# Kernel tuning notes

Measured on AMD Instinct MI355X. Metric: run time of the kernel, lower is better.

The kernel has to match this reference:

```python
import jax, jax.numpy as jnp
import numpy as np

NEG = -1e30

def setup_inputs() -> dict:
    key = jax.random.key(0)
    ks = jax.random.split(key, 11)
    B, NA, NB = 8, 2048, 2048
    in_A, in_B, out_dim = 256, 256, 64
    s = 0.05
    return {
        "h_A": jax.random.normal(ks[0], (B, NA, in_A), jnp.float32),
        "h_B": jax.random.normal(ks[1], (B, NB, in_B), jnp.float32),
        "mask": jax.random.bernoulli(ks[2], 0.5, (B, NA, NB)),
        "WA_w": jax.random.normal(ks[3], (in_A, out_dim), jnp.float32) * s,
        "WA_b": jax.random.normal(ks[4], (out_dim,), jnp.float32) * s,
        "WB_w": jax.random.normal(ks[5], (in_B, out_dim), jnp.float32) * s,
        "WB_b": jax.random.normal(ks[6], (out_dim,), jnp.float32) * s,
        "aA_w": jax.random.normal(ks[7], (out_dim,), jnp.float32) * s,
        "aA_b": jax.random.normal(ks[8], (), jnp.float32) * s,
        "aB_w": jax.random.normal(ks[9], (out_dim,), jnp.float32) * s,
        "aB_b": jax.random.normal(ks[10], (), jnp.float32) * s,
    }

def reference(h_A, h_B, mask, WA_w, WA_b, WB_w, WB_b, aA_w, aA_b, aB_w, aB_b):
    # Linear projections: z_A [B,NA,D], z_B [B,NB,D]
    z_A = jnp.einsum('bnd,df->bnf', h_A, WA_w) + WA_b
    z_B = jnp.einsum('bmd,df->bmf', h_B, WB_w) + WB_b
    # Additive attention scores: [B,NA,1] + [B,1,NB] -> [B,NA,NB]
    sA = z_A @ aA_w + aA_b  # [B,NA]
    sB = z_B @ aB_w + aB_b  # [B,NB]
    e = sA[:, :, None] + sB[:, None, :]
    e = jnp.where(mask, e, NEG)
    e = jax.nn.leaky_relu(e, negative_slope=0.01)
    alpha = jax.nn.softmax(e, axis=-1)
    alpha = jnp.where(mask, alpha, 0.0)
    # Weighted sum over neighbors
    return jnp.einsum('bnm,bmf->bnf', alpha, z_B)
```

## Files before the change

kernel.cpp:

```cpp
#include <hip/hip_runtime.h>

typedef short bf16x8 __attribute__((ext_vector_type(8)));
typedef float f32x4 __attribute__((ext_vector_type(4)));

__device__ __forceinline__ unsigned short f2bf(float x) {
  unsigned u = __float_as_uint(x);
  u += 0x7FFFu + ((u >> 16) & 1u);
  return (unsigned short)(u >> 16);
}
__device__ __forceinline__ float bf2f(unsigned short h) {
  return __uint_as_float(((unsigned)h) << 16);
}

__device__ __forceinline__ float wave_reduce_sum(float v) {
  #pragma unroll
  for (int off = 1; off < 64; off <<= 1) v += __shfl_xor(v, off, 64);
  return v;
}

__global__ void prep_kernel(const float* __restrict__ WA_w, const float* __restrict__ WA_b,
                            const float* __restrict__ aA_w, const float* __restrict__ aA_b,
                            const float* __restrict__ WB_w,
                            const unsigned char* __restrict__ mask8,
                            float* __restrict__ vA, float* __restrict__ cA,
                            unsigned short* __restrict__ WBT, int* __restrict__ mflag) {
  if (blockIdx.x < 64) {
    const int f = blockIdx.x, k = threadIdx.x;
    WBT[f * 256 + k] = f2bf(WB_w[k * 64 + f]);
    return;
  }
  const int t = threadIdx.x;
  const unsigned v = mask8[t * 4 + 1];
  const unsigned long long bal = __ballot(v != 0);
  __shared__ unsigned red[4];
  const int wave = t >> 6, lane = t & 63;
  if (lane == 0) red[wave] = (bal != 0ull) ? 1u : 0u;
  float sa = 0.f;
  for (int ff = 0; ff < 64; ++ff) sa += WA_w[t * 64 + ff] * aA_w[ff];
  vA[t] = sa;
  __syncthreads();
  if (t == 0) {
    float ca = aA_b[0];
    for (int ff = 0; ff < 64; ++ff) ca += WA_b[ff] * aA_w[ff];
    cA[0] = ca;
    mflag[0] = (red[0] | red[1] | red[2] | red[3]) ? 1 : 0;
  }
}

__global__ __launch_bounds__(256) void zB_kernel(
    const float* __restrict__ hB, const unsigned short* __restrict__ WBT,
    const float* __restrict__ WB_b, const float* __restrict__ aB_w,
    const float* __restrict__ aB_b,
    unsigned short* __restrict__ zBT, float* __restrict__ sB,
    float* __restrict__ msB_blk) {
  __shared__ char hl[32768];
  __shared__ char wt[32768];
  __shared__ float red16[16];
  const int t = threadIdx.x, w = t >> 6, l = t & 63;
  const int q = l >> 4, ln = l & 15;
  const int r0 = blockIdx.x * 64;
  const int b = r0 >> 11;
  const int mloc = r0 & 2047;

  {
    const int f = t >> 2, c = t & 3;
    const unsigned short* src = WBT + f * 256;
    #pragma unroll
    for (int j = 0; j < 8; ++j) {
      const int k8 = c + j * 4;
      bf16x8 v = *(const bf16x8*)(src + k8 * 8);
      *(bf16x8*)(wt + ((f * 512 + k8 * 16) ^ ((f & 7) << 4))) = v;
    }
  }
  {
    const int row = t >> 2, seg = t & 3;
    const float* src = hB + (size_t)(r0 + row) * 256 + seg * 64;
    #pragma unroll
    for (int i = 0; i < 8; ++i) {
      float4 x = *(const float4*)(src + i * 8);
      float4 y = *(const float4*)(src + i * 8 + 4);
      bf16x8 v;
      v[0] = (short)f2bf(x.x); v[1] = (short)f2bf(x.y);
      v[2] = (short)f2bf(x.z); v[3] = (short)f2bf(x.w);
      v[4] = (short)f2bf(y.x); v[5] = (short)f2bf(y.y);
      v[6] = (short)f2bf(y.z); v[7] = (short)f2bf(y.w);
      *(bf16x8*)(hl + ((row * 512 + seg * 128 + i * 16) ^ ((row & 7) << 4))) = v;
    }
  }
  __syncthreads();
  f32x4 acc[4];
  #pragma unroll
  for (int nr = 0; nr < 4; ++nr) acc[nr] = (f32x4){0.f, 0.f, 0.f, 0.f};
  const int rowA = w * 16 + ln;
  #pragma unroll
  for (int kk = 0; kk < 8; ++kk) {
    const int ko = kk * 64 + q * 16;
    bf16x8 a = *(const bf16x8*)(hl + ((rowA * 512 + ko) ^ ((rowA & 7) << 4)));
    #pragma unroll
    for (int nr = 0; nr < 4; ++nr) {
      const int f = nr * 16 + ln;
      bf16x8 bb = *(const bf16x8*)(wt + ((f * 512 + ko) ^ ((f & 7) << 4)));
      acc[nr] = __builtin_amdgcn_mfma_f32_16x16x32_bf16(a, bb, acc[nr], 0, 0, 0);
    }
  }
  float z[4][4];
  float p[4] = {0.f, 0.f, 0.f, 0.f};
  #pragma unroll
  for (int nr = 0; nr < 4; ++nr) {
    const int f = nr * 16 + ln;
    const float bias = WB_b[f];
    const float aw = aB_w[f];
    #pragma unroll
    for (int r = 0; r < 4; ++r) {
      const float zz = acc[nr][r] + bias;
      z[nr][r] = zz;
      p[r] += zz * aw;
    }
  }
  #pragma unroll
  for (int r = 0; r < 4; ++r) {
    #pragma unroll
    for (int off = 1; off < 16; off <<= 1) p[r] += __shfl_xor(p[r], off, 16);
  }
  if (ln == 0) {
    const float cb = aB_b[0];
    float lm = -1e30f;
    #pragma unroll
    for (int r = 0; r < 4; ++r) {
      const float s = p[r] + cb;
      sB[r0 + w * 16 + q * 4 + r] = s;
      lm = fmaxf(lm, s);
    }
    red16[w * 4 + q] = lm;
  }
  __syncthreads();
  if (t == 0) {
    float bm = red16[0];
    #pragma unroll
    for (int i = 1; i < 16; ++i) bm = fmaxf(bm, red16[i]);
    msB_blk[blockIdx.x] = bm;
  }
  #pragma unroll
  for (int nr = 0; nr < 4; ++nr) {
    const int f = nr * 16 + ln;
    uint2 pk;
    pk.x = (unsigned)f2bf(z[nr][0]) | ((unsigned)f2bf(z[nr][1]) << 16);
    pk.y = (unsigned)f2bf(z[nr][2]) | ((unsigned)f2bf(z[nr][3]) << 16);
    *(uint2*)(hl + ((f * 128 + (w * 16 + q * 4) * 2) ^ ((f & 7) << 4))) = pk;
  }
  __syncthreads();
  {
    const int sf = t >> 3, sm8 = t & 7;
    #pragma unroll
    for (int i = 0; i < 2; ++i) {
      const int f = sf + i * 32;
      bf16x8 v = *(const bf16x8*)(hl + ((f * 128 + sm8 * 16) ^ ((f & 7) << 4)));
      *(bf16x8*)(zBT + (size_t)b * 131072 + f * 2048 + mloc + sm8 * 8) = v;
    }
  }
}

__global__ __launch_bounds__(256) void gat_kernel(
    const unsigned short* __restrict__ zBT, const float* __restrict__ hA,
    const float* __restrict__ vA, const float* __restrict__ cA,
    const float* __restrict__ sB, const float* __restrict__ msB_blk,
    const unsigned char* __restrict__ mask8, const int* __restrict__ mask32,
    const int* __restrict__ mflag, float* __restrict__ out) {
  const int b = blockIdx.y;
  const int n0 = blockIdx.x * 32;
  const int t = threadIdx.x;
  const int w = t >> 6, l = t & 63;
  const int q = l >> 4, ln = l & 15;
  const bool use8 = (*mflag != 0);

  __shared__ char zbl[2][16384];
  __shared__ char wl[2][8192];
  __shared__ float sAl[32];
  __shared__ float dl[32];

  const float4 vA4 = ((const float4*)vA)[l];
  const float cA0 = cA[0];
  #pragma unroll
  for (int r = 0; r < 8; ++r) {
    const int row = w * 8 + r;
    const float4 h4 = *(const float4*)(hA + ((size_t)(b * 2048 + n0 + row)) * 256 + l * 4);
    float s = h4.x * vA4.x + h4.y * vA4.y + h4.z * vA4.z + h4.w * vA4.w;
    s = wave_reduce_sum(s);
    if (l == 0) sAl[row] = s + cA0;
  }
  float mb = -1e30f;
  #pragma unroll 8
  for (int i = 0; i < 32; ++i) mb = fmaxf(mb, msB_blk[b * 32 + i]);
  __syncthreads();

  const int n2 = t >> 4;
  const int m8 = t & 15;
  const float sA0 = sAl[n2], sA1 = sAl[n2 + 16];
  const float M0f = sA0 + mb, M1f = sA1 + mb;
  const float M0 = M0f >= 0.f ? M0f : 0.01f * M0f;
  const float M1 = M1f >= 0.f ? M1f : 0.01f * M1f;
  float ds0 = 0.f, ds1 = 0.f;
  f32x4 acc0 = (f32x4){0.f, 0.f, 0.f, 0.f}, acc1 = acc0;

  const unsigned short* zb = zBT + (size_t)b * 131072;
  const size_t mrow0 = ((size_t)(b * 2048 + n0 + n2)) * 2048 + m8 * 8;
  const size_t mrow1 = mrow0 + (size_t)16 * 2048;
  const int zf = t >> 2, zseg = t & 3;
  const int fB = w * 16 + ln;
  const int wbyte0 = (n2 * 256 + m8 * 16) ^ ((n2 & 7) << 4);
  const int wbyte1 = ((n2 + 16) * 256 + m8 * 16) ^ (((n2 + 16) & 7) << 4);

  for (int mt = 0; mt < 16; ++mt) {
    const int m0 = mt * 128;
    char* zc = zbl[mt & 1];
    char* wc = wl[mt & 1];
    bf16x8 zv[4];
    #pragma unroll
    for (int i = 0; i < 4; ++i)
      zv[i] = *(const bf16x8*)(zb + zf * 2048 + m0 + zseg * 32 + i * 8);
    const float4 s0 = *(const float4*)(sB + b * 2048 + m0 + m8 * 8);
    const float4 s1 = *(const float4*)(sB + b * 2048 + m0 + m8 * 8 + 4);
    const float sbx[8] = {s0.x, s0.y, s0.z, s0.w, s1.x, s1.y, s1.z, s1.w};
    int k0[8], k1[8];
    if (use8) {
      const uint2 a = *(const uint2*)(mask8 + mrow0 + m0);
      const uint2 c = *(const uint2*)(mask8 + mrow1 + m0);
      #pragma unroll
      for (int j = 0; j < 4; ++j) {
        k0[j] = (a.x >> (8 * j)) & 0xFF; k0[j + 4] = (a.y >> (8 * j)) & 0xFF;
        k1[j] = (c.x >> (8 * j)) & 0xFF; k1[j + 4] = (c.y >> (8 * j)) & 0xFF;
      }
    } else {
      const int4 a = *(const int4*)(mask32 + mrow0 + m0);
      const int4 a2 = *(const int4*)(mask32 + mrow0 + m0 + 4);
      const int4 c = *(const int4*)(mask32 + mrow1 + m0);
      const int4 c2 = *(const int4*)(mask32 + mrow1 + m0 + 4);
      k0[0] = a.x; k0[1] = a.y; k0[2] = a.z; k0[3] = a.w;
      k0[4] = a2.x; k0[5] = a2.y; k0[6] = a2.z; k0[7] = a2.w;
      k1[0] = c.x; k1[1] = c.y; k1[2] = c.z; k1[3] = c.w;
      k1[4] = c2.x; k1[5] = c2.y; k1[6] = c2.z; k1[7] = c2.w;
    }
    unsigned short wb0[8], wb1[8];
    #pragma unroll
    for (int j = 0; j < 8; ++j) {
      const float x0 = sA0 + sbx[j];
      const float e0 = x0 >= 0.f ? x0 : 0.01f * x0;
      const float v0 = k0[j] ? __expf(e0 - M0) : 0.f;
      wb0[j] = f2bf(v0); ds0 += bf2f(wb0[j]);
      const float x1 = sA1 + sbx[j];
      const float e1 = x1 >= 0.f ? x1 : 0.01f * x1;
      const float v1 = k1[j] ? __expf(e1 - M1) : 0.f;
      wb1[j] = f2bf(v1); ds1 += bf2f(wb1[j]);
    }
    #pragma unroll
    for (int i = 0; i < 4; ++i)
      *(bf16x8*)(zc + ((zf * 256 + zseg * 64 + i * 16) ^ ((zf & 7) << 4))) = zv[i];
    uint4 pk0, pk1;
    pk0.x = (unsigned)wb0[0] | ((unsigned)wb0[1] << 16);
    pk0.y = (unsigned)wb0[2] | ((unsigned)wb0[3] << 16);
    pk0.z = (unsigned)wb0[4] | ((unsigned)wb0[5] << 16);
    pk0.w = (unsigned)wb0[6] | ((unsigned)wb0[7] << 16);
    pk1.x = (unsigned)wb1[0] | ((unsigned)wb1[1] << 16);
    pk1.y = (unsigned)wb1[2] | ((unsigned)wb1[3] << 16);
    pk1.z = (unsigned)wb1[4] | ((unsigned)wb1[5] << 16);
    pk1.w = (unsigned)wb1[6] | ((unsigned)wb1[7] << 16);
    *(uint4*)(wc + wbyte0) = pk0;
    *(uint4*)(wc + wbyte1) = pk1;
    __syncthreads();
    #pragma unroll
    for (int kk = 0; kk < 4; ++kk) {
      const int ko = kk * 64 + q * 16;
      bf16x8 bb = *(const bf16x8*)(zc + ((fB * 256 + ko) ^ ((fB & 7) << 4)));
      bf16x8 a0 = *(const bf16x8*)(wc + ((ln * 256 + ko) ^ ((ln & 7) << 4)));
      bf16x8 a1 = *(const bf16x8*)(wc + (((16 + ln) * 256 + ko) ^ (((16 + ln) & 7) << 4)));
      acc0 = __builtin_amdgcn_mfma_f32_16x16x32_bf16(a0, bb, acc0, 0, 0, 0);
      acc1 = __builtin_amdgcn_mfma_f32_16x16x32_bf16(a1, bb, acc1, 0, 0, 0);
    }
  }
  #pragma unroll
  for (int off = 1; off < 16; off <<= 1) {
    ds0 += __shfl_xor(ds0, off, 16);
    ds1 += __shfl_xor(ds1, off, 16);
  }
  if (m8 == 0) { dl[n2] = ds0; dl[n2 + 16] = ds1; }
  __syncthreads();
  #pragma unroll
  for (int r = 0; r < 4; ++r) {
    {
      const int n = q * 4 + r;
      const float d = dl[n];
      out[((size_t)(b * 2048 + n0 + n)) * 64 + w * 16 + ln] = d > 0.f ? acc0[r] / d : 0.f;
    }
    {
      const int n = 16 + q * 4 + r;
      const float d = dl[n];
      out[((size_t)(b * 2048 + n0 + n)) * 64 + w * 16 + ln] = d > 0.f ? acc1[r] / d : 0.f;
    }
  }
}

extern "C" void kernel_launch(void* const* d_in, const int* in_sizes, int n_in,
                              void* d_out, int out_size, void* d_ws, size_t ws_size,
                              hipStream_t stream) {
  const float* h_A = (const float*)d_in[0];
  const float* h_B = (const float*)d_in[1];
  const unsigned char* mask8 = (const unsigned char*)d_in[2];
  const int* mask32 = (const int*)d_in[2];
  const float* WA_w = (const float*)d_in[3];
  const float* WA_b = (const float*)d_in[4];
  const float* WB_w = (const float*)d_in[5];
  const float* WB_b = (const float*)d_in[6];
  const float* aA_w = (const float*)d_in[7];
  const float* aA_b = (const float*)d_in[8];
  const float* aB_w = (const float*)d_in[9];
  const float* aB_b = (const float*)d_in[10];
  float* out = (float*)d_out;

  char* wsb = (char*)d_ws;
  unsigned short* zBT = (unsigned short*)wsb;
  unsigned short* WBT = (unsigned short*)(wsb + 2097152);
  float* sB      = (float*)(wsb + 2129920);
  float* vA      = (float*)(wsb + 2195456);
  float* cA      = (float*)(wsb + 2196480);
  float* msB_blk = (float*)(wsb + 2196484);
  int* mflag     = (int*)(wsb + 2197508);

  prep_kernel<<<65, 256, 0, stream>>>(WA_w, WA_b, aA_w, aA_b, WB_w, mask8,
                                      vA, cA, WBT, mflag);
  zB_kernel<<<256, 256, 0, stream>>>(h_B, WBT, WB_b, aB_w, aB_b, zBT, sB, msB_blk);
  gat_kernel<<<dim3(64, 8), 256, 0, stream>>>(zBT, h_A, vA, cA, sB, msB_blk,
                                              mask8, mask32, mflag, out);
}
```

Measured before the change: 63.95 us.

## Drop prep kernel, fuse prep into consumers, software-pipeline GAT loads

Removes the separate prep kernel. WB_w transposition moves into the zB kernel, and the vA/cA/mask-format detection moves into the GAT kernel prologue, saving one launch. The zB kernel now uses 32-row tiles over 512 blocks, and each block re-converts the full weight matrix. The GAT kernel goes to 512 threads with one row per thread group, stages sB in LDS, and register-prefetches the next tile's zB and mask loads while computing the current one. The cost is redundant per-block weight work and higher register and LDS pressure.

After: 59.30 us. 1.08x faster.

```diff
diff --git a/kernel.cpp b/kernel.cpp
--- a/kernel.cpp
+++ b/kernel.cpp
@@ -12,108 +12,73 @@
   return __uint_as_float(((unsigned)h) << 16);
 }
 
-__device__ __forceinline__ float wave_reduce_sum(float v) {
-  #pragma unroll
-  for (int off = 1; off < 64; off <<= 1) v += __shfl_xor(v, off, 64);
-  return v;
-}
-
-__global__ void prep_kernel(const float* __restrict__ WA_w, const float* __restrict__ WA_b,
-                            const float* __restrict__ aA_w, const float* __restrict__ aA_b,
-                            const float* __restrict__ WB_w,
-                            const unsigned char* __restrict__ mask8,
-                            float* __restrict__ vA, float* __restrict__ cA,
-                            unsigned short* __restrict__ WBT, int* __restrict__ mflag) {
-  if (blockIdx.x < 64) {
-    const int f = blockIdx.x, k = threadIdx.x;
-    WBT[f * 256 + k] = f2bf(WB_w[k * 64 + f]);
-    return;
-  }
-  const int t = threadIdx.x;
-  const unsigned v = mask8[t * 4 + 1];
-  const unsigned long long bal = __ballot(v != 0);
-  __shared__ unsigned red[4];
-  const int wave = t >> 6, lane = t & 63;
-  if (lane == 0) red[wave] = (bal != 0ull) ? 1u : 0u;
-  float sa = 0.f;
-  for (int ff = 0; ff < 64; ++ff) sa += WA_w[t * 64 + ff] * aA_w[ff];
-  vA[t] = sa;
-  __syncthreads();
-  if (t == 0) {
-    float ca = aA_b[0];
-    for (int ff = 0; ff < 64; ++ff) ca += WA_b[ff] * aA_w[ff];
-    cA[0] = ca;
-    mflag[0] = (red[0] | red[1] | red[2] | red[3]) ? 1 : 0;
-  }
-}
-
-__global__ __launch_bounds__(256) void zB_kernel(
-    const float* __restrict__ hB, const unsigned short* __restrict__ WBT,
+__global__ __launch_bounds__(256) void zb_kernel(
+    const float* __restrict__ hB, const float* __restrict__ WB_w,
     const float* __restrict__ WB_b, const float* __restrict__ aB_w,
     const float* __restrict__ aB_b,
     unsigned short* __restrict__ zBT, float* __restrict__ sB,
     float* __restrict__ msB_blk) {
-  __shared__ char hl[32768];
   __shared__ char wt[32768];
-  __shared__ float red16[16];
+  __shared__ char hl[16384];
+  __shared__ float redp[4][16];
+  __shared__ float sred[32];
+
   const int t = threadIdx.x, w = t >> 6, l = t & 63;
   const int q = l >> 4, ln = l & 15;
-  const int r0 = blockIdx.x * 64;
-  const int b = r0 >> 11;
-  const int mloc = r0 & 2047;
+  const int m0g = blockIdx.x * 32;
+  const int b = m0g >> 11, mloc = m0g & 2047;
 
   {
-    const int f = t >> 2, c = t & 3;
-    const unsigned short* src = WBT + f * 256;
+    const int f = t >> 2, kseg = t & 3;
     #pragma unroll
     for (int j = 0; j < 8; ++j) {
-      const int k8 = c + j * 4;
-      bf16x8 v = *(const bf16x8*)(src + k8 * 8);
-      *(bf16x8*)(wt + ((f * 512 + k8 * 16) ^ ((f & 7) << 4))) = v;
+      const int k0 = kseg * 64 + j * 8;
+      bf16x8 v;
+      #pragma unroll
+      for (int jj = 0; jj < 8; ++jj)
+        v[jj] = (short)f2bf(WB_w[(k0 + jj) * 64 + f]);
+      *(bf16x8*)(wt + ((f * 512 + k0 * 2) ^ ((f & 7) << 4))) = v;
     }
   }
   {
-    const int row = t >> 2, seg = t & 3;
-    const float* src = hB + (size_t)(r0 + row) * 256 + seg * 64;
     #pragma unroll
     for (int i = 0; i < 8; ++i) {
-      float4 x = *(const float4*)(src + i * 8);
-      float4 y = *(const float4*)(src + i * 8 + 4);
-      bf16x8 v;
-      v[0] = (short)f2bf(x.x); v[1] = (short)f2bf(x.y);
-      v[2] = (short)f2bf(x.z); v[3] = (short)f2bf(x.w);
-      v[4] = (short)f2bf(y.x); v[5] = (short)f2bf(y.y);
-      v[6] = (short)f2bf(y.z); v[7] = (short)f2bf(y.w);
-      *(bf16x8*)(hl + ((row * 512 + seg * 128 + i * 16) ^ ((row & 7) << 4))) = v;
-    }
-  }
-  __syncthreads();
-  f32x4 acc[4];
-  #pragma unroll
-  for (int nr = 0; nr < 4; ++nr) acc[nr] = (f32x4){0.f, 0.f, 0.f, 0.f};
-  const int rowA = w * 16 + ln;
+      const int idx = i * 1024 + t * 4;
+      const int row = idx >> 8, k = idx & 255;
+      const float4 x = *(const float4*)(hB + (size_t)m0g * 256 + idx);
+      uint2 pk;
+      pk.x = (unsigned)f2bf(x.x) | ((unsigned)f2bf(x.y) << 16);
+      pk.y = (unsigned)f2bf(x.z) | ((unsigned)f2bf(x.w) << 16);
+      *(uint2*)(hl + ((row * 512 + k * 2) ^ ((row & 7) << 4))) = pk;
+    }
+  }
+  __syncthreads();
+  const int rt = w & 1, fpair = w >> 1;
+  f32x4 acc[2];
+  acc[0] = (f32x4){0.f, 0.f, 0.f, 0.f};
+  acc[1] = acc[0];
+  const int rowA = rt * 16 + ln;
   #pragma unroll
   for (int kk = 0; kk < 8; ++kk) {
     const int ko = kk * 64 + q * 16;
-    bf16x8 a = *(const bf16x8*)(hl + ((rowA * 512 + ko) ^ ((rowA & 7) << 4)));
-    #pragma unroll
-    for (int nr = 0; nr < 4; ++nr) {
-      const int f = nr * 16 + ln;
-      bf16x8 bb = *(const bf16x8*)(wt + ((f * 512 + ko) ^ ((f & 7) << 4)));
-      acc[nr] = __builtin_amdgcn_mfma_f32_16x16x32_bf16(a, bb, acc[nr], 0, 0, 0);
-    }
-  }
-  float z[4][4];
+    const bf16x8 a = *(const bf16x8*)(hl + ((rowA * 512 + ko) ^ ((rowA & 7) << 4)));
+    #pragma unroll
+    for (int j = 0; j < 2; ++j) {
+      const int f = fpair * 32 + j * 16 + ln;
+      const bf16x8 bb = *(const bf16x8*)(wt + ((f * 512 + ko) ^ ((f & 7) << 4)));
+      acc[j] = __builtin_amdgcn_mfma_f32_16x16x32_bf16(a, bb, acc[j], 0, 0, 0);
+    }
+  }
+  float z[2][4];
   float p[4] = {0.f, 0.f, 0.f, 0.f};
   #pragma unroll
-  for (int nr = 0; nr < 4; ++nr) {
-    const int f = nr * 16 + ln;
-    const float bias = WB_b[f];
-    const float aw = aB_w[f];
+  for (int j = 0; j < 2; ++j) {
+    const int f = fpair * 32 + j * 16 + ln;
+    const float bias = WB_b[f], aw = aB_w[f];
     #pragma unroll
     for (int r = 0; r < 4; ++r) {
-      const float zz = acc[nr][r] + bias;
-      z[nr][r] = zz;
+      const float zz = acc[j][r] + bias;
+      z[j][r] = zz;
       p[r] += zz * aw;
     }
   }
@@ -123,179 +88,209 @@
     for (int off = 1; off < 16; off <<= 1) p[r] += __shfl_xor(p[r], off, 16);
   }
   if (ln == 0) {
-    const float cb = aB_b[0];
-    float lm = -1e30f;
-    #pragma unroll
-    for (int r = 0; r < 4; ++r) {
-      const float s = p[r] + cb;
-      sB[r0 + w * 16 + q * 4 + r] = s;
-      lm = fmaxf(lm, s);
-    }
-    red16[w * 4 + q] = lm;
+    #pragma unroll
+    for (int r = 0; r < 4; ++r) redp[w][q * 4 + r] = p[r];
+  }
+  __syncthreads();
+  char* zt = hl;
+  #pragma unroll
+  for (int j = 0; j < 2; ++j) {
+    const int f = fpair * 32 + j * 16 + ln;
+    uint2 pk;
+    pk.x = (unsigned)f2bf(z[j][0]) | ((unsigned)f2bf(z[j][1]) << 16);
+    pk.y = (unsigned)f2bf(z[j][2]) | ((unsigned)f2bf(z[j][3]) << 16);
+    *(uint2*)(zt + f * 80 + (rt * 16 + q * 4) * 2) = pk;
+  }
+  if (t < 32) {
+    const int rtm = t >> 4, mi = t & 15;
+    const float s = redp[rtm][mi] + redp[rtm + 2][mi] + aB_b[0];
+    sB[m0g + t] = s;
+    sred[t] = s;
   }
   __syncthreads();
   if (t == 0) {
-    float bm = red16[0];
-    #pragma unroll
-    for (int i = 1; i < 16; ++i) bm = fmaxf(bm, red16[i]);
+    float bm = sred[0];
+    #pragma unroll
+    for (int i = 1; i < 32; ++i) bm = fmaxf(bm, sred[i]);
     msB_blk[blockIdx.x] = bm;
   }
-  #pragma unroll
-  for (int nr = 0; nr < 4; ++nr) {
-    const int f = nr * 16 + ln;
-    uint2 pk;
-    pk.x = (unsigned)f2bf(z[nr][0]) | ((unsigned)f2bf(z[nr][1]) << 16);
-    pk.y = (unsigned)f2bf(z[nr][2]) | ((unsigned)f2bf(z[nr][3]) << 16);
-    *(uint2*)(hl + ((f * 128 + (w * 16 + q * 4) * 2) ^ ((f & 7) << 4))) = pk;
-  }
-  __syncthreads();
   {
-    const int sf = t >> 3, sm8 = t & 7;
-    #pragma unroll
-    for (int i = 0; i < 2; ++i) {
-      const int f = sf + i * 32;
-      bf16x8 v = *(const bf16x8*)(hl + ((f * 128 + sm8 * 16) ^ ((f & 7) << 4)));
-      *(bf16x8*)(zBT + (size_t)b * 131072 + f * 2048 + mloc + sm8 * 8) = v;
-    }
-  }
-}
-
-__global__ __launch_bounds__(256) void gat_kernel(
+    const int f = t >> 2, mseg = t & 3;
+    const bf16x8 v = *(const bf16x8*)(zt + f * 80 + mseg * 16);
+    *(bf16x8*)(zBT + (size_t)b * 131072 + f * 2048 + mloc + mseg * 8) = v;
+  }
+}
+
+struct Pref {
+  bf16x8 za, zb2;
+  uint2 mk;
+  int4 m32a, m32b;
+};
+
+__device__ __forceinline__ void gat_load(Pref& p,
+    const unsigned short* zrow, const unsigned char* mk8, const int* mk32,
+    const bool use8, const int m0) {
+  p.za = *(const bf16x8*)(zrow + m0);
+  p.zb2 = *(const bf16x8*)(zrow + m0 + 8);
+  if (use8) {
+    p.mk = *(const uint2*)(mk8 + m0);
+  } else {
+    p.m32a = *(const int4*)(mk32 + m0);
+    p.m32b = *(const int4*)(mk32 + m0 + 4);
+  }
+}
+
+__device__ __forceinline__ void gat_body(const Pref& p, char* zc, char* wc,
+    const float* sBl, const int m0, const int m8, const float sAr, const float M,
+    const bool use8, const int zw0, const int zw1, const int wbyte, float& ds) {
+  *(bf16x8*)(zc + zw0) = p.za;
+  *(bf16x8*)(zc + zw1) = p.zb2;
+  const int sbase = m0 + m8 * 8;
+  const float4 s0 = *(const float4*)(sBl + sbase);
+  const float4 s1 = *(const float4*)(sBl + sbase + 4);
+  const float sbx[8] = {s0.x, s0.y, s0.z, s0.w, s1.x, s1.y, s1.z, s1.w};
+  int km[8];
+  if (use8) {
+    #pragma unroll
+    for (int j = 0; j < 4; ++j) {
+      km[j] = (p.mk.x >> (8 * j)) & 0xFF;
+      km[j + 4] = (p.mk.y >> (8 * j)) & 0xFF;
+    }
+  } else {
+    km[0] = p.m32a.x; km[1] = p.m32a.y; km[2] = p.m32a.z; km[3] = p.m32a.w;
+    km[4] = p.m32b.x; km[5] = p.m32b.y; km[6] = p.m32b.z; km[7] = p.m32b.w;
+  }
+  unsigned short wb[8];
+  #pragma unroll
+  for (int j = 0; j < 8; ++j) {
+    const float x = sAr + sbx[j];
+    const float e = x >= 0.f ? x : 0.01f * x;
+    const float v = km[j] ? __expf(e - M) : 0.f;
+    wb[j] = f2bf(v);
+    ds += bf2f(wb[j]);
+  }
+  uint4 pk;
+  pk.x = (unsigned)wb[0] | ((unsigned)wb[1] << 16);
+  pk.y = (unsigned)wb[2] | ((unsigned)wb[3] << 16);
+  pk.z = (unsigned)wb[4] | ((unsigned)wb[5] << 16);
+  pk.w = (unsigned)wb[6] | ((unsigned)wb[7] << 16);
+  *(uint4*)(wc + wbyte) = pk;
+}
+
+__device__ __forceinline__ void gat_mfma(const char* zc, const char* wc,
+    f32x4& acc, const int fb, const int ar, const int q) {
+  #pragma unroll
+  for (int kk = 0; kk < 4; ++kk) {
+    const int ko = kk * 64 + q * 16;
+    const bf16x8 bb = *(const bf16x8*)(zc + ((fb * 256 + ko) ^ ((fb & 7) << 4)));
+    const bf16x8 aa = *(const bf16x8*)(wc + ((ar * 256 + ko) ^ ((ar & 7) << 4)));
+    acc = __builtin_amdgcn_mfma_f32_16x16x32_bf16(aa, bb, acc, 0, 0, 0);
+  }
+}
+
+__global__ __launch_bounds__(512, 4) void gat_kernel(
     const unsigned short* __restrict__ zBT, const float* __restrict__ hA,
-    const float* __restrict__ vA, const float* __restrict__ cA,
+    const float* __restrict__ WA_w, const float* __restrict__ WA_b,
+    const float* __restrict__ aA_w, const float* __restrict__ aA_b,
     const float* __restrict__ sB, const float* __restrict__ msB_blk,
     const unsigned char* __restrict__ mask8, const int* __restrict__ mask32,
-    const int* __restrict__ mflag, float* __restrict__ out) {
-  const int b = blockIdx.y;
-  const int n0 = blockIdx.x * 32;
-  const int t = threadIdx.x;
-  const int w = t >> 6, l = t & 63;
+    float* __restrict__ out) {
+  const int b = blockIdx.y, n0 = blockIdx.x * 32;
+  const int t = threadIdx.x, w = t >> 6, l = t & 63;
   const int q = l >> 4, ln = l & 15;
-  const bool use8 = (*mflag != 0);
-
-  __shared__ char zbl[2][16384];
-  __shared__ char wl[2][8192];
+
+  __shared__ char zbl0[16384], zbl1[16384];
+  __shared__ char wl0[8192], wl1[8192];
+  __shared__ float sBl[2048];
+  __shared__ float vAl[256];
   __shared__ float sAl[32];
   __shared__ float dl[32];
-
-  const float4 vA4 = ((const float4*)vA)[l];
-  const float cA0 = cA[0];
-  #pragma unroll
-  for (int r = 0; r < 8; ++r) {
-    const int row = w * 8 + r;
-    const float4 h4 = *(const float4*)(hA + ((size_t)(b * 2048 + n0 + row)) * 256 + l * 4);
-    float s = h4.x * vA4.x + h4.y * vA4.y + h4.z * vA4.z + h4.w * vA4.w;
-    s = wave_reduce_sum(s);
-    if (l == 0) sAl[row] = s + cA0;
-  }
-  float mb = -1e30f;
-  #pragma unroll 8
-  for (int i = 0; i < 32; ++i) mb = fmaxf(mb, msB_blk[b * 32 + i]);
-  __syncthreads();
-
-  const int n2 = t >> 4;
-  const int m8 = t & 15;
-  const float sA0 = sAl[n2], sA1 = sAl[n2 + 16];
-  const float M0f = sA0 + mb, M1f = sA1 + mb;
-  const float M0 = M0f >= 0.f ? M0f : 0.01f * M0f;
-  const float M1 = M1f >= 0.f ? M1f : 0.01f * M1f;
-  float ds0 = 0.f, ds1 = 0.f;
-  f32x4 acc0 = (f32x4){0.f, 0.f, 0.f, 0.f}, acc1 = acc0;
-
-  const unsigned short* zb = zBT + (size_t)b * 131072;
-  const size_t mrow0 = ((size_t)(b * 2048 + n0 + n2)) * 2048 + m8 * 8;
-  const size_t mrow1 = mrow0 + (size_t)16 * 2048;
-  const int zf = t >> 2, zseg = t & 3;
-  const int fB = w * 16 + ln;
-  const int wbyte0 = (n2 * 256 + m8 * 16) ^ ((n2 & 7) << 4);
-  const int wbyte1 = ((n2 + 16) * 256 + m8 * 16) ^ (((n2 + 16) & 7) << 4);
-
-  for (int mt = 0; mt < 16; ++mt) {
-    const int m0 = mt * 128;
-    char* zc = zbl[mt & 1];
-    char* wc = wl[mt & 1];
-    bf16x8 zv[4];
-    #pragma unroll
-    for (int i = 0; i < 4; ++i)
-      zv[i] = *(const bf16x8*)(zb + zf * 2048 + m0 + zseg * 32 + i * 8);
-    const float4 s0 = *(const float4*)(sB + b * 2048 + m0 + m8 * 8);
-    const float4 s1 = *(const float4*)(sB + b * 2048 + m0 + m8 * 8 + 4);
-    const float sbx[8] = {s0.x, s0.y, s0.z, s0.w, s1.x, s1.y, s1.z, s1.w};
-    int k0[8], k1[8];
-    if (use8) {
-      const uint2 a = *(const uint2*)(mask8 + mrow0 + m0);
-      const uint2 c = *(const uint2*)(mask8 + mrow1 + m0);
+  __shared__ float cAl;
+  __shared__ unsigned dfl[4];
+
+  if (t < 256) {
+    const unsigned vdet = mask8[t * 4 + 1];
+    const unsigned long long bal = __ballot(vdet != 0);
+    if (l == 0) dfl[w] = (bal != 0ull) ? 1u : 0u;
+    const float4* wr = (const float4*)(WA_w + t * 64);
+    const float4* a4 = (const float4*)aA_w;
+    float s = 0.f;
+    #pragma unroll
+    for (int i = 0; i < 16; ++i) {
+      const float4 x = wr[i], y = a4[i];
+      s += x.x * y.x + x.y * y.y + x.z * y.z + x.w * y.w;
+    }
+    vAl[t] = s;
+  } else {
+    const int u = t - 256;
+    ((float4*)sBl)[u * 2] = ((const float4*)(sB + b * 2048))[u * 2];
+    ((float4*)sBl)[u * 2 + 1] = ((const float4*)(sB + b * 2048))[u * 2 + 1];
+    if (u == 0) {
+      float ca = aA_b[0];
+      for (int f = 0; f < 64; ++f) ca += WA_b[f] * aA_w[f];
+      cAl = ca;
+    }
+  }
+  float mb = msB_blk[b * 64 + l];
+  #pragma unroll
+  for (int off = 1; off < 64; off <<= 1) mb = fmaxf(mb, __shfl_xor(mb, off, 64));
+  __syncthreads();
+  const bool use8 = (dfl[0] | dfl[1] | dfl[2] | dfl[3]) != 0;
+  {
+    const float4 vA4 = ((const float4*)vAl)[l];
+    const float cA0 = cAl;
+    #pragma unroll
+    for (int rr = 0; rr < 4; ++rr) {
+      const int row = w * 4 + rr;
+      const float4 h4 = *(const float4*)(hA + ((size_t)(b * 2048 + n0 + row)) * 256 + l * 4);
+      float s = h4.x * vA4.x + h4.y * vA4.y + h4.z * vA4.z + h4.w * vA4.w;
       #pragma unroll
-      for (int j = 0; j < 4; ++j) {
-        k0[j] = (a.x >> (8 * j)) & 0xFF; k0[j + 4] = (a.y >> (8 * j)) & 0xFF;
-        k1[j] = (c.x >> (8 * j)) & 0xFF; k1[j + 4] = (c.y >> (8 * j)) & 0xFF;
-      }
-    } else {
-      const int4 a = *(const int4*)(mask32 + mrow0 + m0);
-      const int4 a2 = *(const int4*)(mask32 + mrow0 + m0 + 4);
-      const int4 c = *(const int4*)(mask32 + mrow1 + m0);
-      const int4 c2 = *(const int4*)(mask32 + mrow1 + m0 + 4);
-      k0[0] = a.x; k0[1] = a.y; k0[2] = a.z; k0[3] = a.w;
-      k0[4] = a2.x; k0[5] = a2.y; k0[6] = a2.z; k0[7] = a2.w;
-      k1[0] = c.x; k1[1] = c.y; k1[2] = c.z; k1[3] = c.w;
-      k1[4] = c2.x; k1[5] = c2.y; k1[6] = c2.z; k1[7] = c2.w;
-    }
-    unsigned short wb0[8], wb1[8];
-    #pragma unroll
-    for (int j = 0; j < 8; ++j) {
-      const float x0 = sA0 + sbx[j];
-      const float e0 = x0 >= 0.f ? x0 : 0.01f * x0;
-      const float v0 = k0[j] ? __expf(e0 - M0) : 0.f;
-      wb0[j] = f2bf(v0); ds0 += bf2f(wb0[j]);
-      const float x1 = sA1 + sbx[j];
-      const float e1 = x1 >= 0.f ? x1 : 0.01f * x1;
-      const float v1 = k1[j] ? __expf(e1 - M1) : 0.f;
-      wb1[j] = f2bf(v1); ds1 += bf2f(wb1[j]);
-    }
-    #pragma unroll
-    for (int i = 0; i < 4; ++i)
-      *(bf16x8*)(zc + ((zf * 256 + zseg * 64 + i * 16) ^ ((zf & 7) << 4))) = zv[i];
-    uint4 pk0, pk1;
-    pk0.x = (unsigned)wb0[0] | ((unsigned)wb0[1] << 16);
-    pk0.y = (unsigned)wb0[2] | ((unsigned)wb0[3] << 16);
-    pk0.z = (unsigned)wb0[4] | ((unsigned)wb0[5] << 16);
-    pk0.w = (unsigned)wb0[6] | ((unsigned)wb0[7] << 16);
-    pk1.x = (unsigned)wb1[0] | ((unsigned)wb1[1] << 16);
-    pk1.y = (unsigned)wb1[2] | ((unsigned)wb1[3] << 16);
-    pk1.z = (unsigned)wb1[4] | ((unsigned)wb1[5] << 16);
-    pk1.w = (unsigned)wb1[6] | ((unsigned)wb1[7] << 16);
-    *(uint4*)(wc + wbyte0) = pk0;
-    *(uint4*)(wc + wbyte1) = pk1;
+      for (int off = 1; off < 64; off <<= 1) s += __shfl_xor(s, off, 64);
+      if (l == 0) sAl[row] = s + cA0;
+    }
+  }
+  __syncthreads();
+
+  const int r = t >> 4, m8 = t & 15;
+  const float sAr = sAl[r];
+  const float Mf = sAr + mb;
+  const float M = Mf >= 0.f ? Mf : 0.01f * Mf;
+  float ds = 0.f;
+  f32x4 acc = (f32x4){0.f, 0.f, 0.f, 0.f};
+
+  const int zf = t >> 3, zseg = t & 7;
+  const unsigned short* zrow = zBT + (size_t)b * 131072 + zf * 2048 + zseg * 16;
+  const size_t mrowe = ((size_t)(b * 2048 + n0 + r)) * 2048 + m8 * 8;
+  const unsigned char* mk8 = mask8 + mrowe;
+  const int* mk32 = mask32 + mrowe;
+  const int zbase = zf * 256 + zseg * 32;
+  const int swz = (zf & 7) << 4;
+  const int zw0 = zbase ^ swz, zw1 = (zbase + 16) ^ swz;
+  const int wbyte = (r * 256 + m8 * 16) ^ ((r & 7) << 4);
+  const int fb = (w >> 1) * 16 + ln;
+  const int ar = (w & 1) * 16 + ln;
+
+  Pref pA, pB;
+  gat_load(pA, zrow, mk8, mk32, use8, 0);
+  for (int mt = 0; mt < 16; mt += 2) {
+    gat_load(pB, zrow, mk8, mk32, use8, (mt + 1) * 128);
+    gat_body(pA, zbl0, wl0, sBl, mt * 128, m8, sAr, M, use8, zw0, zw1, wbyte, ds);
     __syncthreads();
-    #pragma unroll
-    for (int kk = 0; kk < 4; ++kk) {
-      const int ko = kk * 64 + q * 16;
-      bf16x8 bb = *(const bf16x8*)(zc + ((fB * 256 + ko) ^ ((fB & 7) << 4)));
-      bf16x8 a0 = *(const bf16x8*)(wc + ((ln * 256 + ko) ^ ((ln & 7) << 4)));
-      bf16x8 a1 = *(const bf16x8*)(wc + (((16 + ln) * 256 + ko) ^ (((16 + ln) & 7) << 4)));
-      acc0 = __builtin_amdgcn_mfma_f32_16x16x32_bf16(a0, bb, acc0, 0, 0, 0);
-      acc1 = __builtin_amdgcn_mfma_f32_16x16x32_bf16(a1, bb, acc1, 0, 0, 0);
-    }
-  }
-  #pragma unroll
-  for (int off = 1; off < 16; off <<= 1) {
-    ds0 += __shfl_xor(ds0, off, 16);
-    ds1 += __shfl_xor(ds1, off, 16);
-  }
-  if (m8 == 0) { dl[n2] = ds0; dl[n2 + 16] = ds1; }
-  __syncthreads();
-  #pragma unroll
-  for (int r = 0; r < 4; ++r) {
-    {
-      const int n = q * 4 + r;
-      const float d = dl[n];
-      out[((size_t)(b * 2048 + n0 + n)) * 64 + w * 16 + ln] = d > 0.f ? acc0[r] / d : 0.f;
-    }
-    {
-      const int n = 16 + q * 4 + r;
-      const float d = dl[n];
-      out[((size_t)(b * 2048 + n0 + n)) * 64 + w * 16 + ln] = d > 0.f ? acc1[r] / d : 0.f;
-    }
+    gat_mfma(zbl0, wl0, acc, fb, ar, q);
+    gat_load(pA, zrow, mk8, mk32, use8, ((mt + 2) & 15) * 128);
+    gat_body(pB, zbl1, wl1, sBl, (mt + 1) * 128, m8, sAr, M, use8, zw0, zw1, wbyte, ds);
+    __syncthreads();
+    gat_mfma(zbl1, wl1, acc, fb, ar, q);
+  }
+  #pragma unroll
+  for (int off = 1; off < 16; off <<= 1) ds += __shfl_xor(ds, off, 16);
+  if (m8 == 0) dl[r] = ds;
+  __syncthreads();
+  #pragma unroll
+  for (int rr = 0; rr < 4; ++rr) {
+    const int n = (w & 1) * 16 + q * 4 + rr;
+    const float d = dl[n];
+    out[((size_t)(b * 2048 + n0 + n)) * 64 + fb] = d > 0.f ? acc[rr] / d : 0.f;
   }
 }
 
@@ -318,16 +313,10 @@
 
   char* wsb = (char*)d_ws;
   unsigned short* zBT = (unsigned short*)wsb;
-  unsigned short* WBT = (unsigned short*)(wsb + 2097152);
-  float* sB      = (float*)(wsb + 2129920);
-  float* vA      = (float*)(wsb + 2195456);
-  float* cA      = (float*)(wsb + 2196480);
-  float* msB_blk = (float*)(wsb + 2196484);
-  int* mflag     = (int*)(wsb + 2197508);
-
-  prep_kernel<<<65, 256, 0, stream>>>(WA_w, WA_b, aA_w, aA_b, WB_w, mask8,
-                                      vA, cA, WBT, mflag);
-  zB_kernel<<<256, 256, 0, stream>>>(h_B, WBT, WB_b, aB_w, aB_b, zBT, sB, msB_blk);
-  gat_kernel<<<dim3(64, 8), 256, 0, stream>>>(zBT, h_A, vA, cA, sB, msB_blk,
-                                              mask8, mask32, mflag, out);
-}
+  float* sB      = (float*)(wsb + 2097152);
+  float* msB_blk = (float*)(wsb + 2162688);
+
+  zb_kernel<<<512, 256, 0, stream>>>(h_B, WB_w, WB_b, aB_w, aB_b, zBT, sB, msB_blk);
+  gat_kernel<<<dim3(64, 8), 512, 0, stream>>>(zBT, h_A, WA_w, WA_b, aA_w, aA_b,
+                                              sB, msB_blk, mask8, mask32, out);
+}
```
